# Kernel optimization log

Hardware: AMD Instinct MI355X
Metric: run time of the kernel (lower is better)

## Reference

```python
import jax, jax.numpy as jnp
import numpy as np

LN_EPS = 1e-5


def _ln(x, g, b):
    m = x.mean(-1, keepdims=True)
    v = ((x - m) ** 2).mean(-1, keepdims=True)
    return (x - m) * jax.lax.rsqrt(v + LN_EPS) * g + b


def setup_inputs() -> dict:
    key = jax.random.key(0)
    ks = jax.random.split(key, 8)
    B, S, T, Ds, Dt, H = 2, 1024, 1024, 128, 64, 64

    def w(k, shp):
        return jax.random.normal(k, shp, dtype=jnp.float32) * 0.05

    return {
        "source_features": jax.random.normal(ks[0], (B, S, Ds), dtype=jnp.float32),
        "target_features": jax.random.normal(ks[1], (B, T, Dt), dtype=jnp.float32),
        # source_adapter: Linear(Ds,H) -> LN(H) -> ReLU -> Linear(H,H)
        "sW1": w(ks[2], (Ds, H)), "sb1": jnp.zeros(H), "sg": jnp.ones(H), "sbeta": jnp.zeros(H),
        "sW2": w(ks[3], (H, H)), "sb2": jnp.zeros(H),
        # target_adapter: Linear(Dt,H) -> LN(H) -> ReLU -> Linear(H,H)
        "tW1": w(ks[4], (Dt, H)), "tb1": jnp.zeros(H), "tg": jnp.ones(H), "tbeta": jnp.zeros(H),
        "tW2": w(ks[5], (H, H)), "tb2": jnp.zeros(H),
        # city_features: Linear(2H,H) -> LN(H) -> ReLU
        "cW": w(ks[6], (2 * H, H)), "cb": jnp.zeros(H), "cg": jnp.ones(H), "cbeta": jnp.zeros(H),
        # similarity_module: Linear(H,1) -> Sigmoid
        "simW": w(ks[7], (H, 1)), "simb": jnp.zeros(1),
    }


def reference(source_features, target_features,
              sW1, sb1, sg, sbeta, sW2, sb2,
              tW1, tb1, tg, tbeta, tW2, tb2,
              cW, cb, cg, cbeta, simW, simb):
    H = sW2.shape[1]
    s_ad = jax.nn.relu(_ln(source_features @ sW1 + sb1, sg, sbeta)) @ sW2 + sb2  # [B,S,H]
    t_ad = jax.nn.relu(_ln(target_features @ tW1 + tb1, tg, tbeta)) @ tW2 + tb2  # [B,T,H]

    # concat order in torch is [target, source] on the last dim; split the
    # Linear(2H,H) weight so the [B,T,S,2H] concat is never materialized.
    cW_t, cW_s = cW[:H], cW[H:]
    pre = (t_ad @ cW_t)[:, :, None, :] + (s_ad @ cW_s)[:, None, :, :] + cb  # [B,T,S,H]
    h = jax.nn.relu(_ln(pre, cg, cbeta))
    scores = jax.nn.sigmoid((h @ simW)[..., 0] + simb[0])  # [B,T,S]

    attn = jax.nn.softmax(scores, axis=-1)
    transferred = jnp.einsum('bts,bsh->bth', attn, s_ad)
    gate = jax.nn.sigmoid(t_ad.mean(-1, keepdims=True))
    adapted = t_ad * (1.0 - gate) + transferred * gate  # hidden_dim == target_dim: no proj
    return adapted, scores
```

## Files before the change

### kernel.cpp

```cpp
#include <hip/hip_runtime.h>
#include <math.h>

#define BN 2
#define SN 1024
#define TN 1024
#define DS 128
#define DT 64
#define HN 64
#define LN_EPS 1e-5f

typedef float v2f __attribute__((ext_vector_type(2)));

__device__ __forceinline__ float wave_sum(float v) {
#pragma unroll
  for (int m = 32; m >= 1; m >>= 1) v += __shfl_xor(v, m, 64);
  return v;
}

__device__ __forceinline__ v2f lo2(float4 v) { v2f r = {v.x, v.y}; return r; }
__device__ __forceinline__ v2f hi2(float4 v) { v2f r = {v.z, v.w}; return r; }

__device__ __forceinline__ float rl(float v, int l) {
  return __int_as_float(__builtin_amdgcn_readlane(__float_as_int(v), l));
}

__global__ __launch_bounds__(256) void k_adapters(
    const float* __restrict__ src, const float* __restrict__ tgt,
    const float* __restrict__ sW1, const float* __restrict__ sb1,
    const float* __restrict__ sg, const float* __restrict__ sbeta,
    const float* __restrict__ sW2, const float* __restrict__ sb2,
    const float* __restrict__ tW1, const float* __restrict__ tb1,
    const float* __restrict__ tg, const float* __restrict__ tbeta,
    const float* __restrict__ tW2, const float* __restrict__ tb2,
    const float* __restrict__ cW, const float* __restrict__ cb,
    float* __restrict__ s_ad, float* __restrict__ sc, float* __restrict__ sstats,
    float* __restrict__ t_ad, float* __restrict__ tc, float* __restrict__ tstats)
{
  __shared__ float xbuf[4][DS];
  __shared__ float rbuf[4][HN];
  int w = threadIdx.x >> 6, lane = threadIdx.x & 63;

  if (blockIdx.x < 512) {
    int row = blockIdx.x * 4 + w;
    xbuf[w][lane]      = src[row * DS + lane];
    xbuf[w][lane + 64] = src[row * DS + 64 + lane];
    float a0 = 0.f, a1 = 0.f, a2_ = 0.f, a3 = 0.f;
#pragma unroll 8
    for (int k = 0; k < DS; k += 4) {
      a0  = fmaf(xbuf[w][k + 0], sW1[(k + 0) * HN + lane], a0);
      a1  = fmaf(xbuf[w][k + 1], sW1[(k + 1) * HN + lane], a1);
      a2_ = fmaf(xbuf[w][k + 2], sW1[(k + 2) * HN + lane], a2_);
      a3  = fmaf(xbuf[w][k + 3], sW1[(k + 3) * HN + lane], a3);
    }
    float h1 = ((a0 + a1) + (a2_ + a3)) + sb1[lane];
    float s1 = wave_sum(h1), s2 = wave_sum(h1 * h1);
    float m = s1 * (1.f / HN);
    float var = s2 * (1.f / HN) - m * m;
    float r = fmaxf(0.f, (h1 - m) * rsqrtf(var + LN_EPS) * sg[lane] + sbeta[lane]);
    rbuf[w][lane] = r;
    float b0 = 0.f, b1 = 0.f, b2 = 0.f, b3 = 0.f;
#pragma unroll 4
    for (int j = 0; j < HN; j += 4) {
      b0 = fmaf(rbuf[w][j + 0], sW2[(j + 0) * HN + lane], b0);
      b1 = fmaf(rbuf[w][j + 1], sW2[(j + 1) * HN + lane], b1);
      b2 = fmaf(rbuf[w][j + 2], sW2[(j + 2) * HN + lane], b2);
      b3 = fmaf(rbuf[w][j + 3], sW2[(j + 3) * HN + lane], b3);
    }
    float a2 = ((b0 + b1) + (b2 + b3)) + sb2[lane];
    s_ad[row * HN + lane] = a2;
    rbuf[w][lane] = a2;
    float c0 = 0.f, c1 = 0.f, c2 = 0.f, c3 = 0.f;
#pragma unroll 4
    for (int j = 0; j < HN; j += 4) {
      c0 = fmaf(rbuf[w][j + 0], cW[(HN + j + 0) * HN + lane], c0);
      c1 = fmaf(rbuf[w][j + 1], cW[(HN + j + 1) * HN + lane], c1);
      c2 = fmaf(rbuf[w][j + 2], cW[(HN + j + 2) * HN + lane], c2);
      c3 = fmaf(rbuf[w][j + 3], cW[(HN + j + 3) * HN + lane], c3);
    }
    float scv = (c0 + c1) + (c2 + c3);
    sc[row * HN + lane] = scv;
    float bs = wave_sum(scv), qs = wave_sum(scv * scv);
    if (lane == 0) { sstats[row * 2] = bs; sstats[row * 2 + 1] = qs; }
  } else {
    int row = (blockIdx.x - 512) * 4 + w;
    xbuf[w][lane] = tgt[row * DT + lane];
    float a0 = 0.f, a1 = 0.f, a2_ = 0.f, a3 = 0.f;
#pragma unroll 4
    for (int k = 0; k < DT; k += 4) {
      a0  = fmaf(xbuf[w][k + 0], tW1[(k + 0) * HN + lane], a0);
      a1  = fmaf(xbuf[w][k + 1], tW1[(k + 1) * HN + lane], a1);
      a2_ = fmaf(xbuf[w][k + 2], tW1[(k + 2) * HN + lane], a2_);
      a3  = fmaf(xbuf[w][k + 3], tW1[(k + 3) * HN + lane], a3);
    }
    float h1 = ((a0 + a1) + (a2_ + a3)) + tb1[lane];
    float s1 = wave_sum(h1), s2 = wave_sum(h1 * h1);
    float m = s1 * (1.f / HN);
    float var = s2 * (1.f / HN) - m * m;
    float r = fmaxf(0.f, (h1 - m) * rsqrtf(var + LN_EPS) * tg[lane] + tbeta[lane]);
    rbuf[w][lane] = r;
    float b0 = 0.f, b1 = 0.f, b2 = 0.f, b3 = 0.f;
#pragma unroll 4
    for (int j = 0; j < HN; j += 4) {
      b0 = fmaf(rbuf[w][j + 0], tW2[(j + 0) * HN + lane], b0);
      b1 = fmaf(rbuf[w][j + 1], tW2[(j + 1) * HN + lane], b1);
      b2 = fmaf(rbuf[w][j + 2], tW2[(j + 2) * HN + lane], b2);
      b3 = fmaf(rbuf[w][j + 3], tW2[(j + 3) * HN + lane], b3);
    }
    float a2 = ((b0 + b1) + (b2 + b3)) + tb2[lane];
    t_ad[row * HN + lane] = a2;
    float asum = wave_sum(a2);
    float gate = 1.f / (1.f + __expf(-asum * (1.f / HN)));
    rbuf[w][lane] = a2;
    float c0 = 0.f, c1 = 0.f, c2 = 0.f, c3 = 0.f;
#pragma unroll 4
    for (int j = 0; j < HN; j += 4) {
      c0 = fmaf(rbuf[w][j + 0], cW[(j + 0) * HN + lane], c0);
      c1 = fmaf(rbuf[w][j + 1], cW[(j + 1) * HN + lane], c1);
      c2 = fmaf(rbuf[w][j + 2], cW[(j + 2) * HN + lane], c2);
      c3 = fmaf(rbuf[w][j + 3], cW[(j + 3) * HN + lane], c3);
    }
    float tcv = ((c0 + c1) + (c2 + c3)) + cb[lane];
    tc[row * HN + lane] = tcv;
    float A = wave_sum(tcv), Q = wave_sum(tcv * tcv);
    if (lane == 0) { tstats[row * 3] = A; tstats[row * 3 + 1] = Q; tstats[row * 3 + 2] = gate; }
  }
}

#define ROWDW 68
__global__ __launch_bounds__(512) void k_scores(
    const float* __restrict__ cg, const float* __restrict__ cbeta,
    const float* __restrict__ simW, const float* __restrict__ simb,
    const float* __restrict__ sc, const float* __restrict__ sstats,
    const float* __restrict__ tc, const float* __restrict__ tstats,
    float* __restrict__ out_scores)
{
  __shared__ float tile[64 * ROWDW];
  int tid = threadIdx.x;
  int w = tid >> 6, lane = tid & 63;
  int sblk = blockIdx.x & 15;
  int tblk = (blockIdx.x >> 4) & 63;
  int b    = blockIdx.x >> 10;
  int t0 = tblk * 16 + w * 2;
  int rt0 = __builtin_amdgcn_readfirstlane(b * TN + t0);
  int rt1 = rt0 + 1;
  int s0 = sblk * 64;

  float A0  = tstats[rt0 * 3 + 0];
  float Qt0 = tstats[rt0 * 3 + 1];
  float A1  = tstats[rt1 * 3 + 0];
  float Qt1 = tstats[rt1 * 3 + 1];
  const float4* tq0 = (const float4*)(tc + rt0 * HN);
  const float4* tq1 = (const float4*)(tc + rt1 * HN);
  const float4* cgq = (const float4*)cg;
  const float4* cbq = (const float4*)cbeta;
  const float4* swq = (const float4*)simW;
  float simb0 = simb[0];

  const float4* scg = (const float4*)(sc + b * SN * HN);

  {
    int r0s = tid >> 4, gs = tid & 15;
    float4 v0 = scg[(s0 + r0s) * 16 + gs];
    float4 v1 = scg[(s0 + r0s + 32) * 16 + gs];
    *(float4*)&tile[r0s * ROWDW + gs * 4] = v0;
    *(float4*)&tile[(r0s + 32) * ROWDW + gs * 4] = v1;
  }
  __syncthreads();

  const v2f zero2 = {0.f, 0.f};
  const float* tb_ = &tile[lane * ROWDW];
  int s = s0 + lane;
  float2 bq = *(const float2*)&sstats[(b * SN + s) * 2];

  v2f D0a = zero2, D0b = zero2, D1a = zero2, D1b = zero2;
#pragma unroll
  for (int g = 0; g < 16; ++g) {
    float4 v = *(const float4*)&tb_[g * 4];
    float4 ta = tq0[g]; float4 tbv = tq1[g];
    D0a = __builtin_elementwise_fma(lo2(ta),  lo2(v), D0a);
    D0b = __builtin_elementwise_fma(hi2(ta),  hi2(v), D0b);
    D1a = __builtin_elementwise_fma(lo2(tbv), lo2(v), D1a);
    D1b = __builtin_elementwise_fma(hi2(tbv), hi2(v), D1b);
  }
  v2f Ds0 = D0a + D0b, Ds1 = D1a + D1b;
  float D_0 = Ds0.x + Ds0.y;
  float D_1 = Ds1.x + Ds1.y;

  float mean0  = (A0 + bq.x) * (1.f / HN);
  float var0   = (Qt0 + bq.y + 2.f * D_0) * (1.f / HN) - mean0 * mean0;
  float alpha0 = rsqrtf(var0 + LN_EPS);
  float mean1  = (A1 + bq.x) * (1.f / HN);
  float var1   = (Qt1 + bq.y + 2.f * D_1) * (1.f / HN) - mean1 * mean1;
  float alpha1 = rsqrtf(var1 + LN_EPS);

  v2f m0 = {mean0, mean0}, a0v = {alpha0, alpha0};
  v2f m1 = {mean1, mean1}, a1v = {alpha1, alpha1};
  v2f dt0a = zero2, dt0b = zero2, dt1a = zero2, dt1b = zero2;

#pragma unroll
  for (int g = 0; g < 16; ++g) {
    float4 v  = *(const float4*)&tb_[g * 4];
    float4 c4 = cgq[g]; float4 b4 = cbq[g]; float4 w4 = swq[g];
    float4 ta = tq0[g]; float4 tbv = tq1[g];
    { v2f u = lo2(v) + lo2(ta);  v2f z = u - m0; v2f P = a0v * lo2(c4);
      v2f n = __builtin_elementwise_fma(z, P, lo2(b4));
      v2f r = __builtin_elementwise_max(n, zero2);
      dt0a = __builtin_elementwise_fma(r, lo2(w4), dt0a); }
    { v2f u = hi2(v) + hi2(ta);  v2f z = u - m0; v2f P = a0v * hi2(c4);
      v2f n = __builtin_elementwise_fma(z, P, hi2(b4));
      v2f r = __builtin_elementwise_max(n, zero2);
      dt0b = __builtin_elementwise_fma(r, hi2(w4), dt0b); }
    { v2f u = lo2(v) + lo2(tbv); v2f z = u - m1; v2f P = a1v * lo2(c4);
      v2f n = __builtin_elementwise_fma(z, P, lo2(b4));
      v2f r = __builtin_elementwise_max(n, zero2);
      dt1a = __builtin_elementwise_fma(r, lo2(w4), dt1a); }
    { v2f u = hi2(v) + hi2(tbv); v2f z = u - m1; v2f P = a1v * hi2(c4);
      v2f n = __builtin_elementwise_fma(z, P, hi2(b4));
      v2f r = __builtin_elementwise_max(n, zero2);
      dt1b = __builtin_elementwise_fma(r, hi2(w4), dt1b); }
  }
  v2f dd0 = dt0a + dt0b, dd1 = dt1a + dt1b;
  float dot0 = dd0.x + dd0.y;
  float dot1 = dd1.x + dd1.y;
  float score0 = 1.f / (1.f + __expf(-(dot0 + simb0)));
  float score1 = 1.f / (1.f + __expf(-(dot1 + simb0)));
  out_scores[rt0 * SN + s] = score0;
  out_scores[rt1 * SN + s] = score1;
}

__global__ __launch_bounds__(256) void k_transfer(
    const float* __restrict__ scores, const float* __restrict__ s_ad,
    const float* __restrict__ t_ad, const float* __restrict__ tstats,
    float* __restrict__ out_adapted)
{
  __shared__ float part[4][4][64];
  __shared__ float esumLDS[4][4];
  int tid = threadIdx.x;
  int w = tid >> 6, lane = tid & 63;
  int tblk = blockIdx.x & 255;
  int b    = blockIdx.x >> 8;
  int rtb  = b * TN + tblk * 4;
  const float* sadb = s_ad + b * SN * HN;

  float acc0 = 0.f, acc1 = 0.f, acc2 = 0.f, acc3 = 0.f;
  float es0 = 0.f, es1 = 0.f, es2 = 0.f, es3 = 0.f;
  int s0w = w * 256;

#pragma unroll
  for (int sub = 0; sub < 4; ++sub) {
    int sbase = s0w + sub * 64;
    float e0 = __expf(scores[(rtb + 0) * SN + sbase + lane]);
    float e1 = __expf(scores[(rtb + 1) * SN + sbase + lane]);
    float e2 = __expf(scores[(rtb + 2) * SN + sbase + lane]);
    float e3 = __expf(scores[(rtb + 3) * SN + sbase + lane]);
    es0 += e0; es1 += e1; es2 += e2; es3 += e3;
    const float* srow = sadb + sbase * HN + lane;
#pragma unroll 16
    for (int si = 0; si < 64; ++si) {
      float sv = srow[si * HN];
      acc0 = fmaf(rl(e0, si), sv, acc0);
      acc1 = fmaf(rl(e1, si), sv, acc1);
      acc2 = fmaf(rl(e2, si), sv, acc2);
      acc3 = fmaf(rl(e3, si), sv, acc3);
    }
  }

  part[w][0][lane] = acc0;
  part[w][1][lane] = acc1;
  part[w][2][lane] = acc2;
  part[w][3][lane] = acc3;
  float t0s = wave_sum(es0), t1s = wave_sum(es1);
  float t2s = wave_sum(es2), t3s = wave_sum(es3);
  if (lane == 0) {
    esumLDS[w][0] = t0s; esumLDS[w][1] = t1s;
    esumLDS[w][2] = t2s; esumLDS[w][3] = t3s;
  }
  __syncthreads();

  int t = w, h = lane;
  float x  = part[0][t][h] + part[1][t][h] + part[2][t][h] + part[3][t][h];
  float es = esumLDS[0][t] + esumLDS[1][t] + esumLDS[2][t] + esumLDS[3][t];
  int rt = rtb + t;
  float tr = x / es;
  float gate = tstats[rt * 3 + 2];
  float tad = t_ad[rt * HN + h];
  out_adapted[rt * HN + h] = tad * (1.f - gate) + tr * gate;
}

extern "C" void kernel_launch(void* const* d_in, const int* in_sizes, int n_in,
                              void* d_out, int out_size, void* d_ws, size_t ws_size,
                              hipStream_t stream) {
  const float* src   = (const float*)d_in[0];
  const float* tgt   = (const float*)d_in[1];
  const float* sW1   = (const float*)d_in[2];
  const float* sb1   = (const float*)d_in[3];
  const float* sg    = (const float*)d_in[4];
  const float* sbeta = (const float*)d_in[5];
  const float* sW2   = (const float*)d_in[6];
  const float* sb2   = (const float*)d_in[7];
  const float* tW1   = (const float*)d_in[8];
  const float* tb1   = (const float*)d_in[9];
  const float* tg    = (const float*)d_in[10];
  const float* tbeta = (const float*)d_in[11];
  const float* tW2   = (const float*)d_in[12];
  const float* tb2   = (const float*)d_in[13];
  const float* cW    = (const float*)d_in[14];
  const float* cb    = (const float*)d_in[15];
  const float* cg    = (const float*)d_in[16];
  const float* cbeta = (const float*)d_in[17];
  const float* simW  = (const float*)d_in[18];
  const float* simb  = (const float*)d_in[19];

  float* ws     = (float*)d_ws;
  float* s_ad   = ws;
  float* sc     = ws + 131072;
  float* sstats = ws + 262144;
  float* t_ad   = ws + 266240;
  float* tc     = ws + 397312;
  float* tstats = ws + 528384;

  float* out_adapted = (float*)d_out;
  float* out_scores  = (float*)d_out + 131072;

  hipLaunchKernelGGL(k_adapters, dim3(1024), dim3(256), 0, stream,
                     src, tgt, sW1, sb1, sg, sbeta, sW2, sb2,
                     tW1, tb1, tg, tbeta, tW2, tb2, cW, cb,
                     s_ad, sc, sstats, t_ad, tc, tstats);
  hipLaunchKernelGGL(k_scores, dim3(BN * 64 * 16), dim3(512), 0, stream,
                     cg, cbeta, simW, simb, sc, sstats, tc, tstats, out_scores);
  hipLaunchKernelGGL(k_transfer, dim3(BN * 256), dim3(256), 0, stream,
                     out_scores, s_ad, t_ad, tstats, out_adapted);
}
```

Measured before the change: 146.6 us.

## Fuse score computation and softmax-weighted transfer into one kernel

Result: slower. 162.5 us (+10.9%).

```diff
diff --git a/kernel.cpp b/kernel.cpp
--- a/kernel.cpp
+++ b/kernel.cpp
@@ -127,141 +127,113 @@
 }
 
 #define ROWDW 68
-__global__ __launch_bounds__(512) void k_scores(
+__global__ __launch_bounds__(256) void k_scores_xfer(
     const float* __restrict__ cg, const float* __restrict__ cbeta,
     const float* __restrict__ simW, const float* __restrict__ simb,
     const float* __restrict__ sc, const float* __restrict__ sstats,
     const float* __restrict__ tc, const float* __restrict__ tstats,
-    float* __restrict__ out_scores)
+    const float* __restrict__ s_ad, const float* __restrict__ t_ad,
+    float* __restrict__ out_scores, float* __restrict__ out_adapted)
 {
   __shared__ float tile[64 * ROWDW];
+  __shared__ float eLDS[4][64];
+  __shared__ float part[4][4][64];
+  __shared__ float esumLDS[4];
+
   int tid = threadIdx.x;
-  int w = tid >> 6, lane = tid & 63;
-  int sblk = blockIdx.x & 15;
-  int tblk = (blockIdx.x >> 4) & 63;
-  int b    = blockIdx.x >> 10;
-  int t0 = tblk * 16 + w * 2;
-  int rt0 = __builtin_amdgcn_readfirstlane(b * TN + t0);
-  int rt1 = rt0 + 1;
-  int s0 = sblk * 64;
-
-  float A0  = tstats[rt0 * 3 + 0];
-  float Qt0 = tstats[rt0 * 3 + 1];
-  float A1  = tstats[rt1 * 3 + 0];
-  float Qt1 = tstats[rt1 * 3 + 1];
-  const float4* tq0 = (const float4*)(tc + rt0 * HN);
-  const float4* tq1 = (const float4*)(tc + rt1 * HN);
+  int w = __builtin_amdgcn_readfirstlane(tid >> 6);
+  int lane = tid & 63;
+  int tblk = blockIdx.x & 255;
+  int b    = blockIdx.x >> 8;
+  int rtb  = b * TN + tblk * 4;
+  int rt   = rtb + w;
+
+  const float4* tq = (const float4*)(tc + rt * HN);
+  float4 tcr[16];
+#pragma unroll
+  for (int g = 0; g < 16; ++g) tcr[g] = tq[g];
+  float A = tstats[rt * 3 + 0];
+  float Q = tstats[rt * 3 + 1];
+
   const float4* cgq = (const float4*)cg;
   const float4* cbq = (const float4*)cbeta;
   const float4* swq = (const float4*)simW;
   float simb0 = simb[0];
-
   const float4* scg = (const float4*)(sc + b * SN * HN);
-
-  {
-    int r0s = tid >> 4, gs = tid & 15;
-    float4 v0 = scg[(s0 + r0s) * 16 + gs];
-    float4 v1 = scg[(s0 + r0s + 32) * 16 + gs];
-    *(float4*)&tile[r0s * ROWDW + gs * 4] = v0;
-    *(float4*)&tile[(r0s + 32) * ROWDW + gs * 4] = v1;
-  }
-  __syncthreads();
-
+  const float*  sadb = s_ad + b * SN * HN;
+  const float*  ssb  = sstats + b * SN * 2;
+
+  float acc0 = 0.f, acc1 = 0.f, acc2 = 0.f, acc3 = 0.f;
+  float esacc = 0.f;
+  int r0 = tid >> 4, gs = tid & 15;
   const v2f zero2 = {0.f, 0.f};
-  const float* tb_ = &tile[lane * ROWDW];
-  int s = s0 + lane;
-  float2 bq = *(const float2*)&sstats[(b * SN + s) * 2];
-
-  v2f D0a = zero2, D0b = zero2, D1a = zero2, D1b = zero2;
-#pragma unroll
-  for (int g = 0; g < 16; ++g) {
-    float4 v = *(const float4*)&tb_[g * 4];
-    float4 ta = tq0[g]; float4 tbv = tq1[g];
-    D0a = __builtin_elementwise_fma(lo2(ta),  lo2(v), D0a);
-    D0b = __builtin_elementwise_fma(hi2(ta),  hi2(v), D0b);
-    D1a = __builtin_elementwise_fma(lo2(tbv), lo2(v), D1a);
-    D1b = __builtin_elementwise_fma(hi2(tbv), hi2(v), D1b);
-  }
-  v2f Ds0 = D0a + D0b, Ds1 = D1a + D1b;
-  float D_0 = Ds0.x + Ds0.y;
-  float D_1 = Ds1.x + Ds1.y;
-
-  float mean0  = (A0 + bq.x) * (1.f / HN);
-  float var0   = (Qt0 + bq.y + 2.f * D_0) * (1.f / HN) - mean0 * mean0;
-  float alpha0 = rsqrtf(var0 + LN_EPS);
-  float mean1  = (A1 + bq.x) * (1.f / HN);
-  float var1   = (Qt1 + bq.y + 2.f * D_1) * (1.f / HN) - mean1 * mean1;
-  float alpha1 = rsqrtf(var1 + LN_EPS);
-
-  v2f m0 = {mean0, mean0}, a0v = {alpha0, alpha0};
-  v2f m1 = {mean1, mean1}, a1v = {alpha1, alpha1};
-  v2f dt0a = zero2, dt0b = zero2, dt1a = zero2, dt1b = zero2;
-
-#pragma unroll
-  for (int g = 0; g < 16; ++g) {
-    float4 v  = *(const float4*)&tb_[g * 4];
-    float4 c4 = cgq[g]; float4 b4 = cbq[g]; float4 w4 = swq[g];
-    float4 ta = tq0[g]; float4 tbv = tq1[g];
-    { v2f u = lo2(v) + lo2(ta);  v2f z = u - m0; v2f P = a0v * lo2(c4);
-      v2f n = __builtin_elementwise_fma(z, P, lo2(b4));
-      v2f r = __builtin_elementwise_max(n, zero2);
-      dt0a = __builtin_elementwise_fma(r, lo2(w4), dt0a); }
-    { v2f u = hi2(v) + hi2(ta);  v2f z = u - m0; v2f P = a0v * hi2(c4);
-      v2f n = __builtin_elementwise_fma(z, P, hi2(b4));
-      v2f r = __builtin_elementwise_max(n, zero2);
-      dt0b = __builtin_elementwise_fma(r, hi2(w4), dt0b); }
-    { v2f u = lo2(v) + lo2(tbv); v2f z = u - m1; v2f P = a1v * lo2(c4);
-      v2f n = __builtin_elementwise_fma(z, P, lo2(b4));
-      v2f r = __builtin_elementwise_max(n, zero2);
-      dt1a = __builtin_elementwise_fma(r, lo2(w4), dt1a); }
-    { v2f u = hi2(v) + hi2(tbv); v2f z = u - m1; v2f P = a1v * hi2(c4);
-      v2f n = __builtin_elementwise_fma(z, P, hi2(b4));
-      v2f r = __builtin_elementwise_max(n, zero2);
-      dt1b = __builtin_elementwise_fma(r, hi2(w4), dt1b); }
-  }
-  v2f dd0 = dt0a + dt0b, dd1 = dt1a + dt1b;
-  float dot0 = dd0.x + dd0.y;
-  float dot1 = dd1.x + dd1.y;
-  float score0 = 1.f / (1.f + __expf(-(dot0 + simb0)));
-  float score1 = 1.f / (1.f + __expf(-(dot1 + simb0)));
-  out_scores[rt0 * SN + s] = score0;
-  out_scores[rt1 * SN + s] = score1;
-}
-
-__global__ __launch_bounds__(256) void k_transfer(
-    const float* __restrict__ scores, const float* __restrict__ s_ad,
-    const float* __restrict__ t_ad, const float* __restrict__ tstats,
-    float* __restrict__ out_adapted)
-{
-  __shared__ float part[4][4][64];
-  __shared__ float esumLDS[4][4];
-  int tid = threadIdx.x;
-  int w = tid >> 6, lane = tid & 63;
-  int tblk = blockIdx.x & 255;
-  int b    = blockIdx.x >> 8;
-  int rtb  = b * TN + tblk * 4;
-  const float* sadb = s_ad + b * SN * HN;
-
-  float acc0 = 0.f, acc1 = 0.f, acc2 = 0.f, acc3 = 0.f;
-  float es0 = 0.f, es1 = 0.f, es2 = 0.f, es3 = 0.f;
-  int s0w = w * 256;
-
-#pragma unroll
-  for (int sub = 0; sub < 4; ++sub) {
-    int sbase = s0w + sub * 64;
-    float e0 = __expf(scores[(rtb + 0) * SN + sbase + lane]);
-    float e1 = __expf(scores[(rtb + 1) * SN + sbase + lane]);
-    float e2 = __expf(scores[(rtb + 2) * SN + sbase + lane]);
-    float e3 = __expf(scores[(rtb + 3) * SN + sbase + lane]);
-    es0 += e0; es1 += e1; es2 += e2; es3 += e3;
-    const float* srow = sadb + sbase * HN + lane;
-#pragma unroll 16
-    for (int si = 0; si < 64; ++si) {
+
+  for (int chunk = 0; chunk < 16; ++chunk) {
+    int s0 = chunk * 64;
+    {
+      float4 v0 = scg[(s0 + r0)      * 16 + gs];
+      float4 v1 = scg[(s0 + r0 + 16) * 16 + gs];
+      float4 v2 = scg[(s0 + r0 + 32) * 16 + gs];
+      float4 v3 = scg[(s0 + r0 + 48) * 16 + gs];
+      *(float4*)&tile[(r0)      * ROWDW + gs * 4] = v0;
+      *(float4*)&tile[(r0 + 16) * ROWDW + gs * 4] = v1;
+      *(float4*)&tile[(r0 + 32) * ROWDW + gs * 4] = v2;
+      *(float4*)&tile[(r0 + 48) * ROWDW + gs * 4] = v3;
+    }
+    __syncthreads();
+
+    const float* tb_ = &tile[lane * ROWDW];
+    float2 bq = *(const float2*)&ssb[(s0 + lane) * 2];
+    float4 v[16];
+    v2f Da = zero2, Db = zero2;
+#pragma unroll
+    for (int g = 0; g < 16; ++g) {
+      v[g] = *(const float4*)&tb_[g * 4];
+      Da = __builtin_elementwise_fma(lo2(tcr[g]), lo2(v[g]), Da);
+      Db = __builtin_elementwise_fma(hi2(tcr[g]), hi2(v[g]), Db);
+    }
+    v2f Ds = Da + Db;
+    float D_ = Ds.x + Ds.y;
+
+    float mean  = (A + bq.x) * (1.f / HN);
+    float var   = (Q + bq.y + 2.f * D_) * (1.f / HN) - mean * mean;
+    float alpha = rsqrtf(var + LN_EPS);
+    v2f mv = {mean, mean}, av = {alpha, alpha};
+    v2f da = zero2, db = zero2;
+
+#pragma unroll
+    for (int g = 0; g < 16; ++g) {
+      float4 c4 = cgq[g]; float4 b4 = cbq[g]; float4 w4 = swq[g];
+      { v2f u = lo2(v[g]) + lo2(tcr[g]); v2f z = u - mv; v2f P = av * lo2(c4);
+        v2f n = __builtin_elementwise_fma(z, P, lo2(b4));
+        v2f r = __builtin_elementwise_max(n, zero2);
+        da = __builtin_elementwise_fma(r, lo2(w4), da); }
+      { v2f u = hi2(v[g]) + hi2(tcr[g]); v2f z = u - mv; v2f P = av * hi2(c4);
+        v2f n = __builtin_elementwise_fma(z, P, hi2(b4));
+        v2f r = __builtin_elementwise_max(n, zero2);
+        db = __builtin_elementwise_fma(r, hi2(w4), db); }
+    }
+    v2f dd = da + db;
+    float dot = dd.x + dd.y;
+    float score = 1.f / (1.f + __expf(-(dot + simb0)));
+    out_scores[rt * SN + s0 + lane] = score;
+
+    float e = __expf(score);
+    esacc += e;
+    eLDS[w][lane] = e;
+    __syncthreads();
+
+    float e0 = eLDS[0][lane], e1 = eLDS[1][lane];
+    float e2 = eLDS[2][lane], e3 = eLDS[3][lane];
+    const float* srow = sadb + (s0 + w * 16) * HN + lane;
+#pragma unroll
+    for (int si = 0; si < 16; ++si) {
       float sv = srow[si * HN];
-      acc0 = fmaf(rl(e0, si), sv, acc0);
-      acc1 = fmaf(rl(e1, si), sv, acc1);
-      acc2 = fmaf(rl(e2, si), sv, acc2);
-      acc3 = fmaf(rl(e3, si), sv, acc3);
+      int l = w * 16 + si;
+      acc0 = fmaf(rl(e0, l), sv, acc0);
+      acc1 = fmaf(rl(e1, l), sv, acc1);
+      acc2 = fmaf(rl(e2, l), sv, acc2);
+      acc3 = fmaf(rl(e3, l), sv, acc3);
     }
   }
 
@@ -269,22 +241,18 @@
   part[w][1][lane] = acc1;
   part[w][2][lane] = acc2;
   part[w][3][lane] = acc3;
-  float t0s = wave_sum(es0), t1s = wave_sum(es1);
-  float t2s = wave_sum(es2), t3s = wave_sum(es3);
-  if (lane == 0) {
-    esumLDS[w][0] = t0s; esumLDS[w][1] = t1s;
-    esumLDS[w][2] = t2s; esumLDS[w][3] = t3s;
-  }
+  float es = wave_sum(esacc);
+  if (lane == 0) esumLDS[w] = es;
   __syncthreads();
 
-  int t = w, h = lane;
-  float x  = part[0][t][h] + part[1][t][h] + part[2][t][h] + part[3][t][h];
-  float es = esumLDS[0][t] + esumLDS[1][t] + esumLDS[2][t] + esumLDS[3][t];
-  int rt = rtb + t;
-  float tr = x / es;
-  float gate = tstats[rt * 3 + 2];
-  float tad = t_ad[rt * HN + h];
-  out_adapted[rt * HN + h] = tad * (1.f - gate) + tr * gate;
+  int tt = w, h = lane;
+  float x   = part[0][tt][h] + part[1][tt][h] + part[2][tt][h] + part[3][tt][h];
+  float esd = esumLDS[tt];
+  int rt2 = rtb + tt;
+  float tr   = x / esd;
+  float gate = tstats[rt2 * 3 + 2];
+  float tad  = t_ad[rt2 * HN + h];
+  out_adapted[rt2 * HN + h] = tad * (1.f - gate) + tr * gate;
 }
 
 extern "C" void kernel_launch(void* const* d_in, const int* in_sizes, int n_in,
@@ -326,8 +294,7 @@
                      src, tgt, sW1, sb1, sg, sbeta, sW2, sb2,
                      tW1, tb1, tg, tbeta, tW2, tb2, cW, cb,
                      s_ad, sc, sstats, t_ad, tc, tstats);
-  hipLaunchKernelGGL(k_scores, dim3(BN * 64 * 16), dim3(512), 0, stream,
-                     cg, cbeta, simW, simb, sc, sstats, tc, tstats, out_scores);
-  hipLaunchKernelGGL(k_transfer, dim3(BN * 256), dim3(256), 0, stream,
-                     out_scores, s_ad, t_ad, tstats, out_adapted);
-}
+  hipLaunchKernelGGL(k_scores_xfer, dim3(BN * 256), dim3(256), 0, stream,
+                     cg, cbeta, simW, simb, sc, sstats, tc, tstats,
+                     s_ad, t_ad, out_scores, out_adapted);
+}
```
